# Kernel optimization log

Hardware: AMD Instinct MI355X
Metric: run time of the kernel (lower is better)

## Reference

```python
import jax, jax.numpy as jnp
import numpy as np

F1, F2 = 256, 128
N1, N2 = 85, 5625
E1, E2 = 1360, 180000


def gcn_conv(x, edge_index, W, b, n):
    """PyG GCNConv: D^{-1/2}(A+I)D^{-1/2} X W + b with unit edge weights."""
    h = x @ W  # [n, out]
    loop = jnp.arange(n)
    src = jnp.concatenate([edge_index[0], loop])
    dst = jnp.concatenate([edge_index[1], loop])
    ones = jnp.ones(src.shape[0], dtype=h.dtype)
    deg = jax.ops.segment_sum(ones, dst, num_segments=n)
    dinv = jnp.where(deg > 0, deg ** -0.5, 0.0)
    norm = dinv[src] * dinv[dst]  # [E+n]
    out = jax.ops.segment_sum(h[src] * norm[:, None], dst, num_segments=n)
    return out + b


def setup_inputs() -> dict:
    key = jax.random.key(0)
    ks = jax.random.split(key, 10)
    x1 = jax.random.normal(ks[0], (N1, F1), dtype=jnp.float32)
    x2 = jax.random.normal(ks[1], (N2, F2), dtype=jnp.float32)
    edge_index1 = jax.random.randint(ks[2], (2, E1), 0, N1)
    edge_index2 = jax.random.randint(ks[3], (2, E2), 0, N2)
    # GCNConv weights (glorot-ish scale) and biases
    W1 = jax.random.normal(ks[4], (F1, 200), dtype=jnp.float32) / np.sqrt(F1)
    b1 = jnp.zeros((200,), dtype=jnp.float32)
    W2 = jax.random.normal(ks[5], (F2, 2), dtype=jnp.float32) / np.sqrt(F2)
    b2 = jnp.zeros((2,), dtype=jnp.float32)
    # final Linear(113, 5)
    Wf = jax.random.normal(ks[6], (113, 5), dtype=jnp.float32) / np.sqrt(113)
    bf = jnp.zeros((5,), dtype=jnp.float32)
    return {"x1": x1, "x2": x2, "W1": W1, "b1": b1, "W2": W2, "b2": b2,
            "Wf": Wf, "bf": bf, "edge_index1": edge_index1, "edge_index2": edge_index2}


def reference(x1, x2, W1, b1, W2, b2, Wf, bf, edge_index1, edge_index2):
    h1 = gcn_conv(x1, edge_index1, W1, b1, N1)          # [85, 200]
    h1 = h1.reshape(250, 68)
    h2 = gcn_conv(x2, edge_index2, W2, b2, N2)          # [5625, 2]
    h2 = h2.reshape(250, 45)
    h = jnp.concatenate([h1, h2], axis=1)               # [250, 113]
    h = jax.nn.relu(h)
    return h @ Wf + bf                                   # [250, 5]
```

## Files before the change

### kernel.cpp

```cpp
#include <hip/hip_runtime.h>

constexpr int cN1 = 85,  cF1 = 256, cO1 = 200, cE1 = 1360;
constexpr int cN2 = 5625, cF2 = 128, cE2 = 180000;

constexpr int NPART = 8;
constexpr int PBINS = 5632;
constexpr int EPP   = cE2 / NPART;

constexpr int NS  = 90;
constexpr int ESL = cE2 / NS;

constexpr int OFF_PART  = 0;
constexpr int OFF_P2    = NPART * PBINS;
constexpr int OFF_DINV  = OFF_P2 + NS * PBINS * 2;
constexpr int OFF_HS2   = OFF_DINV + PBINS;
constexpr int OFF_DINV1 = OFF_HS2 + PBINS * 2;
constexpr int OFF_G1    = OFF_DINV1 + 128;
constexpr int OFF_H1    = OFF_G1 + cN1 * cO1;

constexpr int KA_GRID = NPART + 1 + cN1;

__global__ __launch_bounds__(256) void kA_hist_gemm1(
    const float* __restrict__ x1, const float* __restrict__ W1,
    const int* __restrict__ ei1, const int* __restrict__ ei2,
    float* __restrict__ ws_f)
{
    int* ws_i = reinterpret_cast<int*>(ws_f);
    int b = blockIdx.x, t = threadIdx.x;

    if (b < NPART) {
        __shared__ int s_h[PBINS];
        for (int i = t; i < PBINS; i += 256) s_h[i] = 0;
        __syncthreads();
        const int* dstp = ei2 + cE2 + b * EPP;
        #pragma unroll 4
        for (int i = t; i < EPP; i += 256)
            atomicAdd(&s_h[dstp[i]], 1);
        __syncthreads();
        for (int i = t; i < PBINS; i += 256)
            ws_i[OFF_PART + b * PBINS + i] = s_h[i];
        return;
    }
    b -= NPART;

    if (b == 0) {
        __shared__ int s_deg[cN1];
        if (t < cN1) s_deg[t] = 0;
        __syncthreads();
        for (int i = t; i < cE1; i += 256) atomicAdd(&s_deg[ei1[cE1 + i]], 1);
        __syncthreads();
        if (t < cN1) ws_f[OFF_DINV1 + t] = rsqrtf((float)(s_deg[t] + 1));
        return;
    }
    b -= 1;

    if (t < cO1) {
        const float* xr = x1 + b * cF1;
        float s = 0.f;
        #pragma unroll 16
        for (int k = 0; k < cF1; ++k)
            s = fmaf(xr[k], W1[k * cO1 + t], s);
        ws_f[OFF_H1 + b * cO1 + t] = s;
    }
}

constexpr int KB_GRID = (cN2 + 7) / 8;

__global__ __launch_bounds__(256) void kB_gemm2_table(
    const float* __restrict__ x2, const float* __restrict__ W2,
    float* __restrict__ ws_f)
{
    const int* ws_i = reinterpret_cast<const int*>(ws_f);
    int b = blockIdx.x, t = threadIdx.x;
    int row = b * 8 + (t >> 5), l = t & 31;
    if (row >= cN2) return;

    float4 xv = reinterpret_cast<const float4*>(x2 + row * cF2)[l];
    int kb = l * 4;
    float p0 = xv.x * W2[(kb + 0) * 2 + 0] + xv.y * W2[(kb + 1) * 2 + 0]
             + xv.z * W2[(kb + 2) * 2 + 0] + xv.w * W2[(kb + 3) * 2 + 0];
    float p1 = xv.x * W2[(kb + 0) * 2 + 1] + xv.y * W2[(kb + 1) * 2 + 1]
             + xv.z * W2[(kb + 2) * 2 + 1] + xv.w * W2[(kb + 3) * 2 + 1];
    #pragma unroll
    for (int m = 16; m >= 1; m >>= 1) {
        p0 += __shfl_xor(p0, m);
        p1 += __shfl_xor(p1, m);
    }
    if (l == 0) {
        int d = 0;
        #pragma unroll
        for (int p = 0; p < NPART; ++p) d += ws_i[OFF_PART + p * PBINS + row];
        float dv = rsqrtf((float)(d + 1));
        ws_f[OFF_DINV + row] = dv;
        reinterpret_cast<float2*>(ws_f + OFF_HS2)[row] =
            make_float2(dv * p0, dv * p1);
    }
}

constexpr int KC_GRID = cN1 + NS;

__global__ __launch_bounds__(256) void kC_gather(
    const int* __restrict__ ei1, const int* __restrict__ ei2,
    float* __restrict__ ws_f)
{
    __shared__ float sm[2 * PBINS];
    int b = blockIdx.x, t = threadIdx.x;

    if (b < cN1) {
        int* s_list = reinterpret_cast<int*>(sm);
        if (t == 0) s_list[0] = 0;
        __syncthreads();
        for (int i = t; i < cE1; i += 256) {
            int d = ei1[cE1 + i];
            if (d == b) {
                int k = atomicAdd(&s_list[0], 1) + 1;
                s_list[k] = ei1[i];
            }
        }
        __syncthreads();
        int cnt = s_list[0];
        if (t < cO1) {
            float acc = 0.f;
            for (int m = 1; m <= cnt; ++m) {
                int s = s_list[m];
                acc = fmaf(ws_f[OFF_DINV1 + s], ws_f[OFF_H1 + s * cO1 + t], acc);
            }
            float dn = ws_f[OFF_DINV1 + b];
            ws_f[OFF_G1 + b * cO1 + t] =
                dn * (acc + dn * ws_f[OFF_H1 + b * cO1 + t]);
        }
        return;
    }
    int s = b - cN1;

    for (int i = t; i < 2 * PBINS; i += 256) sm[i] = 0.f;
    __syncthreads();
    const int e0 = s * ESL;
    #pragma unroll
    for (int batch = 0; batch < 2; ++batch) {
        int off = batch * 1024 + t * 4;
        if (off < ESL) {
            int4 s4 = *reinterpret_cast<const int4*>(ei2 + e0 + off);
            int4 d4 = *reinterpret_cast<const int4*>(ei2 + cE2 + e0 + off);
            const float2* hs2 = reinterpret_cast<const float2*>(ws_f + OFF_HS2);
            float2 h0 = hs2[s4.x], h1 = hs2[s4.y], h2 = hs2[s4.z], h3 = hs2[s4.w];
            atomicAdd(&sm[d4.x * 2 + 0], h0.x); atomicAdd(&sm[d4.x * 2 + 1], h0.y);
            atomicAdd(&sm[d4.y * 2 + 0], h1.x); atomicAdd(&sm[d4.y * 2 + 1], h1.y);
            atomicAdd(&sm[d4.z * 2 + 0], h2.x); atomicAdd(&sm[d4.z * 2 + 1], h2.y);
            atomicAdd(&sm[d4.w * 2 + 0], h3.x); atomicAdd(&sm[d4.w * 2 + 1], h3.y);
        }
    }
    __syncthreads();
    float* dst = ws_f + OFF_P2 + s * PBINS * 2;
    for (int i = t; i < 2 * PBINS; i += 256) dst[i] = sm[i];
}

__global__ __launch_bounds__(128) void kD_head(
    const float* __restrict__ ws_f,
    const float* __restrict__ b1, const float* __restrict__ b2,
    const float* __restrict__ Wf, const float* __restrict__ bf,
    float* __restrict__ out)
{
    __shared__ float sred[45][2];
    __shared__ float sh[113];
    int r = blockIdx.x, t = threadIdx.x;

    if (t < 90) {
        int j = t >> 1, half = t & 1;
        int f = r * 45 + j, n = f >> 1, c = f & 1;
        const float* base = ws_f + OFF_P2 + n * 2 + c;
        float s = 0.f;
        #pragma unroll 9
        for (int p = half * 45; p < half * 45 + 45; ++p)
            s += base[p * PBINS * 2];
        sred[j][half] = s;
    }
    __syncthreads();

    if (t < 113) {
        float v;
        if (t < 68) {
            int f = r * 68 + t;
            v = ws_f[OFF_G1 + f] + b1[f % 200];
        } else {
            int j = t - 68;
            int f = r * 45 + j, n = f >> 1, c = f & 1;
            float sum = ws_f[OFF_HS2 + n * 2 + c]
                      + sred[j][0] + sred[j][1];
            v = ws_f[OFF_DINV + n] * sum + b2[c];
        }
        sh[t] = fmaxf(v, 0.f);
    }
    __syncthreads();

    if (t < 80) {
        int o = t >> 4, l = t & 15;
        float s = 0.f;
        for (int k = l; k < 113; k += 16)
            s = fmaf(sh[k], Wf[k * 5 + o], s);
        #pragma unroll
        for (int m = 8; m >= 1; m >>= 1) s += __shfl_down(s, m, 16);
        if (l == 0) out[r * 5 + o] = s + bf[o];
    }
}

extern "C" void kernel_launch(void* const* d_in, const int* in_sizes, int n_in,
                              void* d_out, int out_size, void* d_ws, size_t ws_size,
                              hipStream_t stream)
{
    const float* x1 = (const float*)d_in[0];
    const float* x2 = (const float*)d_in[1];
    const float* W1 = (const float*)d_in[2];
    const float* b1 = (const float*)d_in[3];
    const float* W2 = (const float*)d_in[4];
    const float* b2 = (const float*)d_in[5];
    const float* Wf = (const float*)d_in[6];
    const float* bf = (const float*)d_in[7];
    const int*   ei1 = (const int*)d_in[8];
    const int*   ei2 = (const int*)d_in[9];
    float* ws_f = (float*)d_ws;
    float* out  = (float*)d_out;

    kA_hist_gemm1<<<KA_GRID, 256, 0, stream>>>(x1, W1, ei1, ei2, ws_f);
    kB_gemm2_table<<<KB_GRID, 256, 0, stream>>>(x2, W2, ws_f);
    kC_gather<<<KC_GRID, 256, 0, stream>>>(ei1, ei2, ws_f);
    kD_head<<<250, 128, 0, stream>>>(ws_f, b1, b2, Wf, bf, out);
}
```

Measured before the change: 34.41 us.

## Merge gemm2 into front kernel and defer degree normalization to gather

The x2@W2 projection no longer depends on the degree histogram, so it moves into the first kernel alongside the histogram and gemm1, which removes one launch. Each gather block now sums the partial histograms into a shared-memory degree table and applies rsqrt source normalization per edge. The head recomputes dinv for the self-loop and destination scaling. The cost is that every one of the 90 gather blocks redundantly reads 8x5625 histogram ints and uses more shared memory.

Result: slower. 36.78 us (+6.9%).

```diff
diff --git a/kernel.cpp b/kernel.cpp
--- a/kernel.cpp
+++ b/kernel.cpp
@@ -12,16 +12,17 @@
 
 constexpr int OFF_PART  = 0;
 constexpr int OFF_P2    = NPART * PBINS;
-constexpr int OFF_DINV  = OFF_P2 + NS * PBINS * 2;
-constexpr int OFF_HS2   = OFF_DINV + PBINS;
-constexpr int OFF_DINV1 = OFF_HS2 + PBINS * 2;
+constexpr int OFF_DINV1 = OFF_P2 + NS * PBINS * 2;
 constexpr int OFF_G1    = OFF_DINV1 + 128;
 constexpr int OFF_H1    = OFF_G1 + cN1 * cO1;
-
-constexpr int KA_GRID = NPART + 1 + cN1;
-
-__global__ __launch_bounds__(256) void kA_hist_gemm1(
-    const float* __restrict__ x1, const float* __restrict__ W1,
+constexpr int OFF_H2    = OFF_H1 + cN1 * cO1;
+
+constexpr int G2_B    = (cN2 + 7) / 8;
+constexpr int K1_GRID = NPART + 1 + cN1 + G2_B;
+
+__global__ __launch_bounds__(256) void k1_front(
+    const float* __restrict__ x1, const float* __restrict__ x2,
+    const float* __restrict__ W1, const float* __restrict__ W2,
     const int* __restrict__ ei1, const int* __restrict__ ei2,
     float* __restrict__ ws_f)
 {
@@ -54,60 +55,49 @@
     }
     b -= 1;
 
-    if (t < cO1) {
-        const float* xr = x1 + b * cF1;
-        float s = 0.f;
-        #pragma unroll 16
-        for (int k = 0; k < cF1; ++k)
-            s = fmaf(xr[k], W1[k * cO1 + t], s);
-        ws_f[OFF_H1 + b * cO1 + t] = s;
-    }
-}
-
-constexpr int KB_GRID = (cN2 + 7) / 8;
-
-__global__ __launch_bounds__(256) void kB_gemm2_table(
-    const float* __restrict__ x2, const float* __restrict__ W2,
-    float* __restrict__ ws_f)
-{
-    const int* ws_i = reinterpret_cast<const int*>(ws_f);
-    int b = blockIdx.x, t = threadIdx.x;
+    if (b < cN1) {
+        if (t < cO1) {
+            const float* xr = x1 + b * cF1;
+            float s = 0.f;
+            #pragma unroll 32
+            for (int k = 0; k < cF1; ++k)
+                s = fmaf(xr[k], W1[k * cO1 + t], s);
+            ws_f[OFF_H1 + b * cO1 + t] = s;
+        }
+        return;
+    }
+    b -= cN1;
+
     int row = b * 8 + (t >> 5), l = t & 31;
-    if (row >= cN2) return;
-
-    float4 xv = reinterpret_cast<const float4*>(x2 + row * cF2)[l];
-    int kb = l * 4;
-    float p0 = xv.x * W2[(kb + 0) * 2 + 0] + xv.y * W2[(kb + 1) * 2 + 0]
-             + xv.z * W2[(kb + 2) * 2 + 0] + xv.w * W2[(kb + 3) * 2 + 0];
-    float p1 = xv.x * W2[(kb + 0) * 2 + 1] + xv.y * W2[(kb + 1) * 2 + 1]
-             + xv.z * W2[(kb + 2) * 2 + 1] + xv.w * W2[(kb + 3) * 2 + 1];
-    #pragma unroll
-    for (int m = 16; m >= 1; m >>= 1) {
-        p0 += __shfl_xor(p0, m);
-        p1 += __shfl_xor(p1, m);
-    }
-    if (l == 0) {
-        int d = 0;
+    if (row < cN2) {
+        float4 xv = reinterpret_cast<const float4*>(x2 + row * cF2)[l];
+        int kb = l * 4;
+        float p0 = xv.x * W2[(kb + 0) * 2 + 0] + xv.y * W2[(kb + 1) * 2 + 0]
+                 + xv.z * W2[(kb + 2) * 2 + 0] + xv.w * W2[(kb + 3) * 2 + 0];
+        float p1 = xv.x * W2[(kb + 0) * 2 + 1] + xv.y * W2[(kb + 1) * 2 + 1]
+                 + xv.z * W2[(kb + 2) * 2 + 1] + xv.w * W2[(kb + 3) * 2 + 1];
         #pragma unroll
-        for (int p = 0; p < NPART; ++p) d += ws_i[OFF_PART + p * PBINS + row];
-        float dv = rsqrtf((float)(d + 1));
-        ws_f[OFF_DINV + row] = dv;
-        reinterpret_cast<float2*>(ws_f + OFF_HS2)[row] =
-            make_float2(dv * p0, dv * p1);
-    }
-}
-
-constexpr int KC_GRID = cN1 + NS;
-
-__global__ __launch_bounds__(256) void kC_gather(
+        for (int m = 16; m >= 1; m >>= 1) {
+            p0 += __shfl_xor(p0, m);
+            p1 += __shfl_xor(p1, m);
+        }
+        if (l == 0)
+            reinterpret_cast<float2*>(ws_f + OFF_H2)[row] = make_float2(p0, p1);
+    }
+}
+
+constexpr int K2_GRID = cN1 + NS;
+
+__global__ __launch_bounds__(256) void k2_gather(
     const int* __restrict__ ei1, const int* __restrict__ ei2,
     float* __restrict__ ws_f)
 {
-    __shared__ float sm[2 * PBINS];
+    __shared__ float          s_acc[2 * PBINS];
+    __shared__ unsigned short s_deg[PBINS];
     int b = blockIdx.x, t = threadIdx.x;
 
     if (b < cN1) {
-        int* s_list = reinterpret_cast<int*>(sm);
+        int* s_list = reinterpret_cast<int*>(s_acc);
         if (t == 0) s_list[0] = 0;
         __syncthreads();
         for (int i = t; i < cE1; i += 256) {
@@ -132,35 +122,53 @@
         return;
     }
     int s = b - cN1;
-
-    for (int i = t; i < 2 * PBINS; i += 256) sm[i] = 0.f;
-    __syncthreads();
+    const int* ws_i = reinterpret_cast<const int*>(ws_f);
+
+    #pragma unroll 2
+    for (int n = t; n < cN2; n += 256) {
+        int d = 0;
+        #pragma unroll
+        for (int p = 0; p < NPART; ++p) d += ws_i[OFF_PART + p * PBINS + n];
+        s_deg[n] = (unsigned short)d;
+    }
+    for (int i = t; i < 2 * PBINS; i += 256) s_acc[i] = 0.f;
+    __syncthreads();
+
     const int e0 = s * ESL;
+    const float2* h2 = reinterpret_cast<const float2*>(ws_f + OFF_H2);
     #pragma unroll
     for (int batch = 0; batch < 2; ++batch) {
         int off = batch * 1024 + t * 4;
         if (off < ESL) {
             int4 s4 = *reinterpret_cast<const int4*>(ei2 + e0 + off);
             int4 d4 = *reinterpret_cast<const int4*>(ei2 + cE2 + e0 + off);
-            const float2* hs2 = reinterpret_cast<const float2*>(ws_f + OFF_HS2);
-            float2 h0 = hs2[s4.x], h1 = hs2[s4.y], h2 = hs2[s4.z], h3 = hs2[s4.w];
-            atomicAdd(&sm[d4.x * 2 + 0], h0.x); atomicAdd(&sm[d4.x * 2 + 1], h0.y);
-            atomicAdd(&sm[d4.y * 2 + 0], h1.x); atomicAdd(&sm[d4.y * 2 + 1], h1.y);
-            atomicAdd(&sm[d4.z * 2 + 0], h2.x); atomicAdd(&sm[d4.z * 2 + 1], h2.y);
-            atomicAdd(&sm[d4.w * 2 + 0], h3.x); atomicAdd(&sm[d4.w * 2 + 1], h3.y);
+            float2 h0 = h2[s4.x], h1 = h2[s4.y], hh2 = h2[s4.z], h3 = h2[s4.w];
+            float v0 = rsqrtf((float)(s_deg[s4.x] + 1));
+            float v1 = rsqrtf((float)(s_deg[s4.y] + 1));
+            float v2 = rsqrtf((float)(s_deg[s4.z] + 1));
+            float v3 = rsqrtf((float)(s_deg[s4.w] + 1));
+            atomicAdd(&s_acc[d4.x * 2 + 0], h0.x * v0);
+            atomicAdd(&s_acc[d4.x * 2 + 1], h0.y * v0);
+            atomicAdd(&s_acc[d4.y * 2 + 0], h1.x * v1);
+            atomicAdd(&s_acc[d4.y * 2 + 1], h1.y * v1);
+            atomicAdd(&s_acc[d4.z * 2 + 0], hh2.x * v2);
+            atomicAdd(&s_acc[d4.z * 2 + 1], hh2.y * v2);
+            atomicAdd(&s_acc[d4.w * 2 + 0], h3.x * v3);
+            atomicAdd(&s_acc[d4.w * 2 + 1], h3.y * v3);
         }
     }
     __syncthreads();
     float* dst = ws_f + OFF_P2 + s * PBINS * 2;
-    for (int i = t; i < 2 * PBINS; i += 256) dst[i] = sm[i];
-}
-
-__global__ __launch_bounds__(128) void kD_head(
+    for (int i = t; i < 2 * PBINS; i += 256) dst[i] = s_acc[i];
+}
+
+__global__ __launch_bounds__(128) void k3_head(
     const float* __restrict__ ws_f,
     const float* __restrict__ b1, const float* __restrict__ b2,
     const float* __restrict__ Wf, const float* __restrict__ bf,
     float* __restrict__ out)
 {
+    const int* ws_i = reinterpret_cast<const int*>(ws_f);
     __shared__ float sred[45][2];
     __shared__ float sh[113];
     int r = blockIdx.x, t = threadIdx.x;
@@ -185,9 +193,12 @@
         } else {
             int j = t - 68;
             int f = r * 45 + j, n = f >> 1, c = f & 1;
-            float sum = ws_f[OFF_HS2 + n * 2 + c]
-                      + sred[j][0] + sred[j][1];
-            v = ws_f[OFF_DINV + n] * sum + b2[c];
+            int d = 0;
+            #pragma unroll
+            for (int p = 0; p < NPART; ++p) d += ws_i[OFF_PART + p * PBINS + n];
+            float dv = rsqrtf((float)(d + 1));
+            float sum = sred[j][0] + sred[j][1];
+            v = dv * sum + dv * dv * ws_f[OFF_H2 + n * 2 + c] + b2[c];
         }
         sh[t] = fmaxf(v, 0.f);
     }
@@ -221,8 +232,7 @@
     float* ws_f = (float*)d_ws;
     float* out  = (float*)d_out;
 
-    kA_hist_gemm1<<<KA_GRID, 256, 0, stream>>>(x1, W1, ei1, ei2, ws_f);
-    kB_gemm2_table<<<KB_GRID, 256, 0, stream>>>(x2, W2, ws_f);
-    kC_gather<<<KC_GRID, 256, 0, stream>>>(ei1, ei2, ws_f);
-    kD_head<<<250, 128, 0, stream>>>(ws_f, b1, b2, Wf, bf, out);
-}
+    k1_front<<<K1_GRID, 256, 0, stream>>>(x1, x2, W1, W2, ei1, ei2, ws_f);
+    k2_gather<<<K2_GRID, 256, 0, stream>>>(ei1, ei2, ws_f);
+    k3_head<<<250, 128, 0, stream>>>(ws_f, b1, b2, Wf, bf, out);
+}
```
